# Kernel tuning notes

Hardware: AMD Instinct MI355X
Metric: run time of the kernel (lower is better)

The kernel has to match this reference:

```python
import jax, jax.numpy as jnp
import numpy as np

N_NODES = 100000
N_EDGES = 3200000
IN_FEATS = 128
HIDDEN = 8
HEADS = 4
OUT_FEATS = 1
NEG_SLOPE = 0.2


def setup_inputs() -> dict:
    key = jax.random.key(0)
    ks = jax.random.split(key, 12)
    x = jax.random.normal(ks[0], (N_NODES, IN_FEATS), dtype=jnp.float32)
    edge_index = jax.random.randint(ks[1], (2, N_EDGES), 0, N_NODES, dtype=jnp.int64)
    # conv1: in=128 -> heads=4, out=8 (concat)
    s1 = 1.0 / np.sqrt(IN_FEATS)
    W1 = jax.random.uniform(ks[2], (IN_FEATS, HEADS * HIDDEN), jnp.float32, -s1, s1)
    att_src1 = jax.random.normal(ks[3], (HEADS, HIDDEN), dtype=jnp.float32) * 0.1
    att_dst1 = jax.random.normal(ks[4], (HEADS, HIDDEN), dtype=jnp.float32) * 0.1
    b1 = jnp.zeros((HEADS * HIDDEN,), jnp.float32)
    # conv2: in=32 -> heads=1, out=1 (no concat)
    s2 = 1.0 / np.sqrt(HEADS * HIDDEN)
    W2 = jax.random.uniform(ks[5], (HEADS * HIDDEN, 1 * OUT_FEATS), jnp.float32, -s2, s2)
    att_src2 = jax.random.normal(ks[6], (1, OUT_FEATS), dtype=jnp.float32) * 0.1
    att_dst2 = jax.random.normal(ks[7], (1, OUT_FEATS), dtype=jnp.float32) * 0.1
    b2 = jnp.zeros((OUT_FEATS,), jnp.float32)
    return {"x": x, "edge_index": edge_index,
            "W1": W1, "att_src1": att_src1, "att_dst1": att_dst1, "b1": b1,
            "W2": W2, "att_src2": att_src2, "att_dst2": att_dst2, "b2": b2}


def gat_conv(x, src, dst, W, a_src, a_dst, b, heads, out_ch, concat):
    """PyG GATConv (eval mode: dropout identity), self-loops already included in src/dst."""
    N = x.shape[0]
    h = (x @ W).reshape(N, heads, out_ch)                 # [N,H,C]
    alpha_s = jnp.sum(h * a_src[None], axis=-1)           # [N,H]
    alpha_d = jnp.sum(h * a_dst[None], axis=-1)           # [N,H]
    e = jax.nn.leaky_relu(alpha_s[src] + alpha_d[dst], NEG_SLOPE)  # [E,H]
    # segment softmax over incoming edges per destination node
    m = jax.ops.segment_max(e, dst, num_segments=N)       # [N,H]; every node has a self-loop
    ex = jnp.exp(e - m[dst])
    denom = jax.ops.segment_sum(ex, dst, num_segments=N)
    alpha = ex / denom[dst]                               # [E,H]
    msg = alpha[:, :, None] * h[src]                      # [E,H,C]
    agg = jax.ops.segment_sum(msg, dst, num_segments=N)   # [N,H,C]
    if concat:
        agg = agg.reshape(N, heads * out_ch)
    else:
        agg = agg.mean(axis=1)
    return agg + b


def reference(x, edge_index, W1, att_src1, att_dst1, b1, W2, att_src2, att_dst2, b2):
    N = x.shape[0]
    loops = jnp.arange(N, dtype=edge_index.dtype)
    src = jnp.concatenate([edge_index[0], loops])
    dst = jnp.concatenate([edge_index[1], loops])
    h = gat_conv(x, src, dst, W1, att_src1, att_dst1, b1, HEADS, HIDDEN, True)
    h = jax.nn.elu(h)
    out = gat_conv(h, src, dst, W2, att_src2, att_dst2, b2, 1, OUT_FEATS, False)
    return out
```

## Files before the change

kernel.cpp:

```cpp
#include <hip/hip_runtime.h>
#include <hip/hip_fp16.h>

#define NEG_SLOPE 0.2f
#define LOG2E 1.4426950408889634f
#define NC 782
#define TILE 6144
#define CAP 4736

__device__ __forceinline__ int uclamp(int i, int n) {
    return ((unsigned)i < (unsigned)n) ? i : 0;
}


__global__ __launch_bounds__(512) void k_msplit(const int* __restrict__ ei, int* __restrict__ gcur,
                                                int* __restrict__ ebin, int E, int N) {
    __shared__ int hist[NC], lpre[NC], lcur[NC];
    __shared__ int tbuf[TILE];
    __shared__ unsigned short tcb[TILE];
    __shared__ int part[512];
    int t = threadIdx.x;
    int tb = blockIdx.x * TILE;
    int nt = E - tb; if (nt > TILE) nt = TILE; if (nt < 0) nt = 0;
    for (int i = t; i < NC; i += 512) { hist[i] = 0; lcur[i] = 0; }
    __syncthreads();
    int sv[12]; short cbv[12];
#pragma unroll
    for (int j = 0; j < 12; ++j) {
        int idx = tb + j * 512 + t;
        int cb = -1, v = 0;
        if (idx < E) {
            int s = uclamp(ei[idx], N), d = uclamp(ei[E + idx], N);
            cb = d >> 7;
            v = (s << 7) | (d & 127);
            atomicAdd(&hist[cb], 1);
        }
        sv[j] = v; cbv[j] = (short)cb;
    }
    __syncthreads();
    int i0 = 2 * t, i1 = 2 * t + 1;
    int h0 = (i0 < NC) ? hist[i0] : 0;
    int h1 = (i1 < NC) ? hist[i1] : 0;
    int a = h0 + h1;
    part[t] = a;
    __syncthreads();
    for (int off = 1; off < 512; off <<= 1) {
        int v = (t >= off) ? part[t - off] : 0;
        __syncthreads();
        part[t] += v;
        __syncthreads();
    }
    int excl = part[t] - a;
    if (i0 < NC) lpre[i0] = excl;
    if (i1 < NC) lpre[i1] = excl + h0;
    __syncthreads();
    for (int i = t; i < NC; i += 512) {
        int h = hist[i];
        if (h) hist[i] = atomicAdd(&gcur[i], h);
    }
    __syncthreads();
#pragma unroll
    for (int j = 0; j < 12; ++j) {
        int cb = cbv[j];
        if (cb >= 0) {
            int slot = lpre[cb] + atomicAdd(&lcur[cb], 1);
            tbuf[slot] = sv[j];
            tcb[slot] = (unsigned short)cb;
        }
    }
    __syncthreads();
    for (int i = t; i < nt; i += 512) {
        int cb = tcb[i];
        int pos = hist[cb] + (i - lpre[cb]);
        if (pos < (cb + 1) * CAP) ebin[pos] = tbuf[i];
    }
}


__global__ __launch_bounds__(512) void k_sortB(const int* __restrict__ gcur, int* __restrict__ ebin,
                                               int* __restrict__ rstart, int* __restrict__ rend,
                                               int N) {
    __shared__ int buf[CAP];
    __shared__ int cnt[128], pre[128], cur[128];
    __shared__ int part[128];
    int b = blockIdx.x, t = threadIdx.x;
    int p0 = b * CAP;
    int n = gcur[b] - p0;
    if (n < 0) n = 0; if (n > CAP) n = CAP;
    if (t < 128) { cnt[t] = 0; cur[t] = 0; }
    __syncthreads();
    for (int i = t; i < n; i += 512) {
        int v = ebin[p0 + i];
        buf[i] = v;
        atomicAdd(&cnt[v & 127], 1);
    }
    __syncthreads();
    if (t < 128) part[t] = cnt[t];
    __syncthreads();
    if (t < 128) {
        for (int off = 1; off < 128; off <<= 1) {
            int v = (t >= off) ? part[t - off] : 0;
            __syncthreads();
            part[t] += v;
            __syncthreads();
        }
    } else {
        for (int off = 1; off < 128; off <<= 1) { __syncthreads(); __syncthreads(); }
    }
    if (t < 128) {
        int a = cnt[t];
        pre[t] = part[t] - a;
        int d = (b << 7) + t;
        if (d < N) {
            rstart[d] = p0 + pre[t];
            rend[d]   = p0 + pre[t] + a;
        }
    }
    __syncthreads();
    for (int i = t; i < n; i += 512) {
        int v = buf[i];
        int dl = v & 127;
        int pos = p0 + pre[dl] + atomicAdd(&cur[dl], 1);
        ebin[pos] = v >> 7;
    }
}


__global__ __launch_bounds__(256) void k_node1(const float* __restrict__ x,
                                               const float* __restrict__ W1,
                                               const float* __restrict__ asw,
                                               const float* __restrict__ adw,
                                               __half* __restrict__ h1h,
                                               float* __restrict__ as1,
                                               float* __restrict__ ad1,
                                               int* __restrict__ gcur, int N) {
    __shared__ float Wl[128 * 32];
    __shared__ float xl[32 * 132];
    __shared__ float als[32], ald[32];
    int t = threadIdx.x;
    if (blockIdx.x < 4) {
        int gi = blockIdx.x * 256 + t;
        if (gi < NC) gcur[gi] = gi * CAP;
    }
    for (int i = t; i < 128 * 32; i += 256) Wl[i] = W1[i];
    if (t < 32) { als[t] = asw[t]; ald[t] = adw[t]; }
    int nbase = blockIdx.x * 32;
    for (int i = t; i < 1024; i += 256) {
        int nd = i >> 5, j = i & 31;
        int node = nbase + nd;
        float4 v = (node < N) ? ((const float4*)(x + (size_t)node * 128))[j]
                              : make_float4(0.f, 0.f, 0.f, 0.f);
        *(float4*)&xl[nd * 132 + j * 4] = v;
    }
    __syncthreads();
    int nl = t >> 3, cq = t & 7;
    int node = nbase + nl;
    float4 acc = make_float4(0.f, 0.f, 0.f, 0.f);
    const float* xr = &xl[nl * 132];
#pragma unroll 8
    for (int k = 0; k < 128; ++k) {
        float xv = xr[k];
        float4 w = *(const float4*)&Wl[k * 32 + cq * 4];
        acc.x += xv * w.x; acc.y += xv * w.y; acc.z += xv * w.z; acc.w += xv * w.w;
    }
    if (node < N) {
        __half2 ha = __floats2half2_rn(acc.x, acc.y);
        __half2 hb = __floats2half2_rn(acc.z, acc.w);
        uint2 u; u.x = *(unsigned*)&ha; u.y = *(unsigned*)&hb;
        ((uint2*)(h1h + (size_t)node * 32))[cq] = u;
        int c4 = cq * 4;
        float vs = acc.x * als[c4] + acc.y * als[c4 + 1] + acc.z * als[c4 + 2] + acc.w * als[c4 + 3];
        float vd = acc.x * ald[c4] + acc.y * ald[c4 + 1] + acc.z * ald[c4 + 2] + acc.w * ald[c4 + 3];
        vs += __shfl_xor(vs, 1);
        vd += __shfl_xor(vd, 1);
        if ((cq & 1) == 0) {
            as1[node * 4 + (cq >> 1)] = vs * LOG2E;
            ad1[node * 4 + (cq >> 1)] = vd * LOG2E;
        }
    }
}


__global__ __launch_bounds__(256) void k_aggr1(const int* __restrict__ rstart, const int* __restrict__ rend,
                                               const int* __restrict__ col,
                                               const __half* __restrict__ h1h,
                                               const float* __restrict__ as1, const float* __restrict__ ad1,
                                               const float* __restrict__ W2,
                                               float* __restrict__ g, int N) {
    int d = (blockIdx.x * 256 + threadIdx.x) >> 6;
    int lane = threadIdx.x & 63;
    if (d >= N) return;
    int slot = lane >> 2, q = lane & 3;
    float myAd = ad1[d * 4 + q];
    int p0 = rstart[d], p1 = rend[d];
    float acc[8];
#pragma unroll
    for (int i = 0; i < 8; ++i) acc[i] = 0.f;
    float ws = 0.f;
    int p = p0 + slot;
    while (p + 16 < p1) {
        int s0 = __builtin_nontemporal_load(&col[p]);
        int s1 = __builtin_nontemporal_load(&col[p + 16]);
        float av0 = as1[s0 * 4 + q];
        float av1 = as1[s1 * 4 + q];
        const __half* h0 = h1h + (size_t)s0 * 32 + q * 8;
        const __half* h1 = h1h + (size_t)s1 * 32 + q * 8;
        uint4 hv0 = *(const uint4*)h0;
        uint4 hv1 = *(const uint4*)h1;
        float e0 = av0 + myAd; e0 = e0 > 0.f ? e0 : NEG_SLOPE * e0;
        float e1 = av1 + myAd; e1 = e1 > 0.f ? e1 : NEG_SLOPE * e1;
        float w0 = exp2f(e0), w1 = exp2f(e1);
        ws += w0 + w1;
        const __half* a0p = (const __half*)&hv0;
        const __half* a1p = (const __half*)&hv1;
#pragma unroll
        for (int i = 0; i < 8; ++i) acc[i] += w0 * (float)a0p[i];
#pragma unroll
        for (int i = 0; i < 8; ++i) acc[i] += w1 * (float)a1p[i];
        p += 32;
    }
    if (p < p1) {
        int s = __builtin_nontemporal_load(&col[p]);
        float av = as1[s * 4 + q];
        uint4 hv = *(const uint4*)(h1h + (size_t)s * 32 + q * 8);
        float e = av + myAd; e = e > 0.f ? e : NEG_SLOPE * e;
        float w = exp2f(e);
        ws += w;
        const __half* ap = (const __half*)&hv;
#pragma unroll
        for (int i = 0; i < 8; ++i) acc[i] += w * (float)ap[i];
    }
#pragma unroll
    for (int m = 4; m <= 32; m <<= 1) {
        ws += __shfl_xor(ws, m);
#pragma unroll
        for (int i = 0; i < 8; ++i) acc[i] += __shfl_xor(acc[i], m);
    }
    {
        float e = as1[d * 4 + q] + myAd;
        e = e > 0.f ? e : NEG_SLOPE * e;
        float w = exp2f(e);
        uint4 hv = *(const uint4*)(h1h + (size_t)d * 32 + q * 8);
        ws += w;
        const __half* ap = (const __half*)&hv;
#pragma unroll
        for (int i = 0; i < 8; ++i) acc[i] += w * (float)ap[i];
    }
    float inv = 1.f / ws;
    float4 w2a = *(const float4*)(W2 + q * 8);
    float4 w2b = *(const float4*)(W2 + q * 8 + 4);
    float gv = 0.f;
#pragma unroll
    for (int i = 0; i < 8; ++i) {
        float val = acc[i] * inv;
        val = val > 0.f ? val : (__expf(val) - 1.f);
        float w2 = (i < 4) ? ((const float*)&w2a)[i] : ((const float*)&w2b)[i - 4];
        gv += val * w2;
    }
    gv += __shfl_xor(gv, 1);
    gv += __shfl_xor(gv, 2);
    if (lane == 0) g[d] = gv;
}


__global__ __launch_bounds__(256) void k_aggr2(const int* __restrict__ rstart, const int* __restrict__ rend,
                                               const int* __restrict__ col,
                                               const float* __restrict__ g,
                                               const float* __restrict__ asw,
                                               const float* __restrict__ adw,
                                               float* __restrict__ out, int N) {
    int tid = blockIdx.x * 256 + threadIdx.x;
    int d = tid >> 3, l = tid & 7;
    if (d >= N) return;
    float asc = asw[0] * LOG2E;
    float adc = adw[0] * LOG2E;
    float gd = g[d];
    float myd = gd * adc;
    int p0 = rstart[d], p1 = rend[d];
    float ws = 0.f, acc = 0.f;
    for (int p = p0 + l; p < p1; p += 8) {
        float gs = g[__builtin_nontemporal_load(&col[p])];
        float e = gs * asc + myd;
        e = e > 0.f ? e : NEG_SLOPE * e;
        float w = exp2f(e);
        ws += w;
        acc += w * gs;
    }
    ws += __shfl_xor(ws, 1); ws += __shfl_xor(ws, 2); ws += __shfl_xor(ws, 4);
    acc += __shfl_xor(acc, 1); acc += __shfl_xor(acc, 2); acc += __shfl_xor(acc, 4);
    if (l == 0) {
        float e = gd * asc + myd;
        e = e > 0.f ? e : NEG_SLOPE * e;
        float w = exp2f(e);
        ws += w;
        acc += w * gd;
        out[d] = acc / ws;
    }
}

extern "C" void kernel_launch(void* const* d_in, const int* in_sizes, int n_in,
                              void* d_out, int out_size, void* d_ws, size_t ws_size,
                              hipStream_t stream) {
    const float* x    = (const float*)d_in[0];
    const int*   ei   = (const int*)d_in[1];
    const float* W1   = (const float*)d_in[2];
    const float* as1w = (const float*)d_in[3];
    const float* ad1w = (const float*)d_in[4];
    const float* W2   = (const float*)d_in[6];
    const float* as2w = (const float*)d_in[7];
    const float* ad2w = (const float*)d_in[8];

    const int N  = in_sizes[0] / 128;
    const int E  = in_sizes[1] / 2;
    const int EB = NC * CAP;

    char* ws = (char*)d_ws;
    size_t off = 0;
    int*    gcur   = (int*)(ws + off);    off += 16384;
    int*    rstart = (int*)(ws + off);    off += (size_t)N * 4;
    int*    rend   = (int*)(ws + off);    off += (size_t)N * 4;
    int*    ebin   = (int*)(ws + off);    off += (size_t)EB * 4;
    __half* h1h    = (__half*)(ws + off); off += (size_t)N * 64;
    float*  as1    = (float*)(ws + off);  off += (size_t)N * 16;
    float*  ad1    = (float*)(ws + off);  off += (size_t)N * 16;
    float*  g      = (float*)(ws + off);  off += (size_t)N * 4;

    k_node1<<<(N + 31) / 32, 256, 0, stream>>>(x, W1, as1w, ad1w, h1h, as1, ad1, gcur, N);
    k_msplit<<<(E + TILE - 1) / TILE, 512, 0, stream>>>(ei, gcur, ebin, E, N);
    k_sortB<<<NC, 512, 0, stream>>>(gcur, ebin, rstart, rend, N);
    k_aggr1<<<(N + 3) / 4, 256, 0, stream>>>(rstart, rend, ebin, h1h, as1, ad1, W2, g, N);
    k_aggr2<<<(N * 8 + 255) / 256, 256, 0, stream>>>(rstart, rend, ebin, g, as2w, ad2w, (float*)d_out, N);
}
```

Baseline: 262.9 us.

## Split layer-1 aggregation into two head-pair passes with halved feature tables

Node features and attention scores are stored as two separate arrays, each holding two heads, and the first-layer aggregation runs as two kernel launches, one per head pair. Each launch accumulates into g, the second by adding to the first's result. The intent is a smaller gather working set per pass (3.2 MB of fp16 features instead of 6.4 MB) so random source-node gathers hit cache more often. The cost is reading the CSR column indices twice, an extra launch, and a read-modify-write of g.

```diff
diff --git a/kernel.cpp b/kernel.cpp
--- a/kernel.cpp
+++ b/kernel.cpp
@@ -129,9 +129,10 @@
                                                const float* __restrict__ W1,
                                                const float* __restrict__ asw,
                                                const float* __restrict__ adw,
-                                               __half* __restrict__ h1h,
-                                               float* __restrict__ as1,
-                                               float* __restrict__ ad1,
+                                               __half* __restrict__ hA,
+                                               __half* __restrict__ hB,
+                                               float* __restrict__ asA, float* __restrict__ asB,
+                                               float* __restrict__ adA, float* __restrict__ adB,
                                                int* __restrict__ gcur, int N) {
     __shared__ float Wl[128 * 32];
     __shared__ float xl[32 * 132];
@@ -166,31 +167,40 @@
         __half2 ha = __floats2half2_rn(acc.x, acc.y);
         __half2 hb = __floats2half2_rn(acc.z, acc.w);
         uint2 u; u.x = *(unsigned*)&ha; u.y = *(unsigned*)&hb;
-        ((uint2*)(h1h + (size_t)node * 32))[cq] = u;
+        __half* hT = (cq < 4) ? hA : hB;
+        ((uint2*)(hT + (size_t)node * 16))[cq & 3] = u;
         int c4 = cq * 4;
         float vs = acc.x * als[c4] + acc.y * als[c4 + 1] + acc.z * als[c4 + 2] + acc.w * als[c4 + 3];
         float vd = acc.x * ald[c4] + acc.y * ald[c4 + 1] + acc.z * ald[c4 + 2] + acc.w * ald[c4 + 3];
         vs += __shfl_xor(vs, 1);
         vd += __shfl_xor(vd, 1);
         if ((cq & 1) == 0) {
-            as1[node * 4 + (cq >> 1)] = vs * LOG2E;
-            ad1[node * 4 + (cq >> 1)] = vd * LOG2E;
-        }
-    }
-}
-
-
-__global__ __launch_bounds__(256) void k_aggr1(const int* __restrict__ rstart, const int* __restrict__ rend,
-                                               const int* __restrict__ col,
-                                               const __half* __restrict__ h1h,
-                                               const float* __restrict__ as1, const float* __restrict__ ad1,
-                                               const float* __restrict__ W2,
-                                               float* __restrict__ g, int N) {
-    int d = (blockIdx.x * 256 + threadIdx.x) >> 6;
+            int head = cq >> 1;
+            float* asT = (head < 2) ? asA : asB;
+            float* adT = (head < 2) ? adA : adB;
+            int hh = head & 1;
+            asT[node * 2 + hh] = vs * LOG2E;
+            adT[node * 2 + hh] = vd * LOG2E;
+        }
+    }
+}
+
+
+template<int ADD>
+__global__ __launch_bounds__(256) void k_aggr1h(const int* __restrict__ rstart, const int* __restrict__ rend,
+                                                const int* __restrict__ col,
+                                                const __half* __restrict__ hX,
+                                                const float* __restrict__ asX, const float* __restrict__ adX,
+                                                const float* __restrict__ W2h,
+                                                float* __restrict__ g, int N) {
+    int wid = (blockIdx.x * 256 + threadIdx.x) >> 6;
     int lane = threadIdx.x & 63;
+    int half = lane >> 5;
+    int d = wid * 2 + half;
     if (d >= N) return;
-    int slot = lane >> 2, q = lane & 3;
-    float myAd = ad1[d * 4 + q];
+    int slot = (lane >> 1) & 15;
+    int hq = lane & 1;
+    float myAd = adX[d * 2 + hq];
     int p0 = rstart[d], p1 = rend[d];
     float acc[8];
 #pragma unroll
@@ -200,14 +210,12 @@
     while (p + 16 < p1) {
         int s0 = __builtin_nontemporal_load(&col[p]);
         int s1 = __builtin_nontemporal_load(&col[p + 16]);
-        float av0 = as1[s0 * 4 + q];
-        float av1 = as1[s1 * 4 + q];
-        const __half* h0 = h1h + (size_t)s0 * 32 + q * 8;
-        const __half* h1 = h1h + (size_t)s1 * 32 + q * 8;
-        uint4 hv0 = *(const uint4*)h0;
-        uint4 hv1 = *(const uint4*)h1;
-        float e0 = av0 + myAd; e0 = e0 > 0.f ? e0 : NEG_SLOPE * e0;
-        float e1 = av1 + myAd; e1 = e1 > 0.f ? e1 : NEG_SLOPE * e1;
+        float a0 = asX[s0 * 2 + hq];
+        float a1 = asX[s1 * 2 + hq];
+        uint4 hv0 = *(const uint4*)(hX + (size_t)s0 * 16 + hq * 8);
+        uint4 hv1 = *(const uint4*)(hX + (size_t)s1 * 16 + hq * 8);
+        float e0 = a0 + myAd; e0 = e0 > 0.f ? e0 : NEG_SLOPE * e0;
+        float e1 = a1 + myAd; e1 = e1 > 0.f ? e1 : NEG_SLOPE * e1;
         float w0 = exp2f(e0), w1 = exp2f(e1);
         ws += w0 + w1;
         const __half* a0p = (const __half*)&hv0;
@@ -218,36 +226,37 @@
         for (int i = 0; i < 8; ++i) acc[i] += w1 * (float)a1p[i];
         p += 32;
     }
-    if (p < p1) {
+    while (p < p1) {
         int s = __builtin_nontemporal_load(&col[p]);
-        float av = as1[s * 4 + q];
-        uint4 hv = *(const uint4*)(h1h + (size_t)s * 32 + q * 8);
+        float av = asX[s * 2 + hq];
+        uint4 hv = *(const uint4*)(hX + (size_t)s * 16 + hq * 8);
         float e = av + myAd; e = e > 0.f ? e : NEG_SLOPE * e;
         float w = exp2f(e);
         ws += w;
         const __half* ap = (const __half*)&hv;
 #pragma unroll
         for (int i = 0; i < 8; ++i) acc[i] += w * (float)ap[i];
-    }
-#pragma unroll
-    for (int m = 4; m <= 32; m <<= 1) {
+        p += 16;
+    }
+#pragma unroll
+    for (int m = 2; m <= 16; m <<= 1) {
         ws += __shfl_xor(ws, m);
 #pragma unroll
         for (int i = 0; i < 8; ++i) acc[i] += __shfl_xor(acc[i], m);
     }
     {
-        float e = as1[d * 4 + q] + myAd;
+        float e = asX[d * 2 + hq] + myAd;
         e = e > 0.f ? e : NEG_SLOPE * e;
         float w = exp2f(e);
-        uint4 hv = *(const uint4*)(h1h + (size_t)d * 32 + q * 8);
+        uint4 hv = *(const uint4*)(hX + (size_t)d * 16 + hq * 8);
         ws += w;
         const __half* ap = (const __half*)&hv;
 #pragma unroll
         for (int i = 0; i < 8; ++i) acc[i] += w * (float)ap[i];
     }
     float inv = 1.f / ws;
-    float4 w2a = *(const float4*)(W2 + q * 8);
-    float4 w2b = *(const float4*)(W2 + q * 8 + 4);
+    float4 w2a = *(const float4*)(W2h + hq * 8);
+    float4 w2b = *(const float4*)(W2h + hq * 8 + 4);
     float gv = 0.f;
 #pragma unroll
     for (int i = 0; i < 8; ++i) {
@@ -257,8 +266,9 @@
         gv += val * w2;
     }
     gv += __shfl_xor(gv, 1);
-    gv += __shfl_xor(gv, 2);
-    if (lane == 0) g[d] = gv;
+    if ((lane & 31) == 0) {
+        if (ADD) g[d] += gv; else g[d] = gv;
+    }
 }
 
 
@@ -319,14 +329,18 @@
     int*    rstart = (int*)(ws + off);    off += (size_t)N * 4;
     int*    rend   = (int*)(ws + off);    off += (size_t)N * 4;
     int*    ebin   = (int*)(ws + off);    off += (size_t)EB * 4;
-    __half* h1h    = (__half*)(ws + off); off += (size_t)N * 64;
-    float*  as1    = (float*)(ws + off);  off += (size_t)N * 16;
-    float*  ad1    = (float*)(ws + off);  off += (size_t)N * 16;
+    __half* hA     = (__half*)(ws + off); off += (size_t)N * 32;
+    __half* hB     = (__half*)(ws + off); off += (size_t)N * 32;
+    float*  asA    = (float*)(ws + off);  off += (size_t)N * 8;
+    float*  asB    = (float*)(ws + off);  off += (size_t)N * 8;
+    float*  adA    = (float*)(ws + off);  off += (size_t)N * 8;
+    float*  adB    = (float*)(ws + off);  off += (size_t)N * 8;
     float*  g      = (float*)(ws + off);  off += (size_t)N * 4;
 
-    k_node1<<<(N + 31) / 32, 256, 0, stream>>>(x, W1, as1w, ad1w, h1h, as1, ad1, gcur, N);
+    k_node1<<<(N + 31) / 32, 256, 0, stream>>>(x, W1, as1w, ad1w, hA, hB, asA, asB, adA, adB, gcur, N);
     k_msplit<<<(E + TILE - 1) / TILE, 512, 0, stream>>>(ei, gcur, ebin, E, N);
     k_sortB<<<NC, 512, 0, stream>>>(gcur, ebin, rstart, rend, N);
-    k_aggr1<<<(N + 3) / 4, 256, 0, stream>>>(rstart, rend, ebin, h1h, as1, ad1, W2, g, N);
+    k_aggr1h<0><<<(N + 7) / 8, 256, 0, stream>>>(rstart, rend, ebin, hA, asA, adA, W2,      g, N);
+    k_aggr1h<1><<<(N + 7) / 8, 256, 0, stream>>>(rstart, rend, ebin, hB, asB, adB, W2 + 16, g, N);
     k_aggr2<<<(N * 8 + 255) / 256, 256, 0, stream>>>(rstart, rend, ebin, g, as2w, ad2w, (float*)d_out, N);
 }
```

New measurement: 285.2 us. 1.08x slower.

## Recompute source attention logits from fp16 features and use half-wave per node

Applied to the files above, without the earlier changes.

The per-node source attention logit array is no longer written by the node kernel. The aggregation kernel instead recomputes it per edge as a dot product of the gathered fp16 features with the attention weights, which removes one random gather per edge and the as1 buffer. The aggregation also moves from one wavefront per destination node to half a wavefront (32 lanes) per node, so each node uses 8 edge slots and grid size doubles in nodes per block. The cost is extra ALU work per edge and logits computed from half-precision features, which slightly changes numerics.

```diff
diff --git a/kernel.cpp b/kernel.cpp
--- a/kernel.cpp
+++ b/kernel.cpp
@@ -127,22 +127,20 @@
 
 __global__ __launch_bounds__(256) void k_node1(const float* __restrict__ x,
                                                const float* __restrict__ W1,
-                                               const float* __restrict__ asw,
                                                const float* __restrict__ adw,
                                                __half* __restrict__ h1h,
-                                               float* __restrict__ as1,
                                                float* __restrict__ ad1,
                                                int* __restrict__ gcur, int N) {
     __shared__ float Wl[128 * 32];
     __shared__ float xl[32 * 132];
-    __shared__ float als[32], ald[32];
+    __shared__ float ald[32];
     int t = threadIdx.x;
     if (blockIdx.x < 4) {
         int gi = blockIdx.x * 256 + t;
         if (gi < NC) gcur[gi] = gi * CAP;
     }
     for (int i = t; i < 128 * 32; i += 256) Wl[i] = W1[i];
-    if (t < 32) { als[t] = asw[t]; ald[t] = adw[t]; }
+    if (t < 32) ald[t] = adw[t];
     int nbase = blockIdx.x * 32;
     for (int i = t; i < 1024; i += 256) {
         int nd = i >> 5, j = i & 31;
@@ -168,12 +166,9 @@
         uint2 u; u.x = *(unsigned*)&ha; u.y = *(unsigned*)&hb;
         ((uint2*)(h1h + (size_t)node * 32))[cq] = u;
         int c4 = cq * 4;
-        float vs = acc.x * als[c4] + acc.y * als[c4 + 1] + acc.z * als[c4 + 2] + acc.w * als[c4 + 3];
         float vd = acc.x * ald[c4] + acc.y * ald[c4 + 1] + acc.z * ald[c4 + 2] + acc.w * ald[c4 + 3];
-        vs += __shfl_xor(vs, 1);
         vd += __shfl_xor(vd, 1);
         if ((cq & 1) == 0) {
-            as1[node * 4 + (cq >> 1)] = vs * LOG2E;
             ad1[node * 4 + (cq >> 1)] = vd * LOG2E;
         }
     }
@@ -183,13 +178,22 @@
 __global__ __launch_bounds__(256) void k_aggr1(const int* __restrict__ rstart, const int* __restrict__ rend,
                                                const int* __restrict__ col,
                                                const __half* __restrict__ h1h,
-                                               const float* __restrict__ as1, const float* __restrict__ ad1,
+                                               const float* __restrict__ ad1,
+                                               const float* __restrict__ asw,
                                                const float* __restrict__ W2,
                                                float* __restrict__ g, int N) {
-    int d = (blockIdx.x * 256 + threadIdx.x) >> 6;
+    int wid = (blockIdx.x * 256 + threadIdx.x) >> 6;
     int lane = threadIdx.x & 63;
+    int half = lane >> 5;
+    int d = wid * 2 + half;
     if (d >= N) return;
-    int slot = lane >> 2, q = lane & 3;
+    int l5 = lane & 31;
+    int slot = l5 >> 2;
+    int q = lane & 3;
+    float4 aA = *(const float4*)(asw + q * 8);
+    float4 aB = *(const float4*)(asw + q * 8 + 4);
+    float as0 = aA.x * LOG2E, as1 = aA.y * LOG2E, as2 = aA.z * LOG2E, as3 = aA.w * LOG2E;
+    float as4 = aB.x * LOG2E, as5 = aB.y * LOG2E, as6 = aB.z * LOG2E, as7 = aB.w * LOG2E;
     float myAd = ad1[d * 4 + q];
     int p0 = rstart[d], p1 = rend[d];
     float acc[8];
@@ -197,54 +201,51 @@
     for (int i = 0; i < 8; ++i) acc[i] = 0.f;
     float ws = 0.f;
     int p = p0 + slot;
-    while (p + 16 < p1) {
+#define DOT8(hp) (as0*(float)(hp)[0] + as1*(float)(hp)[1] + as2*(float)(hp)[2] + as3*(float)(hp)[3] \
+                + as4*(float)(hp)[4] + as5*(float)(hp)[5] + as6*(float)(hp)[6] + as7*(float)(hp)[7])
+    while (p + 8 < p1) {
         int s0 = __builtin_nontemporal_load(&col[p]);
-        int s1 = __builtin_nontemporal_load(&col[p + 16]);
-        float av0 = as1[s0 * 4 + q];
-        float av1 = as1[s1 * 4 + q];
-        const __half* h0 = h1h + (size_t)s0 * 32 + q * 8;
-        const __half* h1 = h1h + (size_t)s1 * 32 + q * 8;
-        uint4 hv0 = *(const uint4*)h0;
-        uint4 hv1 = *(const uint4*)h1;
-        float e0 = av0 + myAd; e0 = e0 > 0.f ? e0 : NEG_SLOPE * e0;
-        float e1 = av1 + myAd; e1 = e1 > 0.f ? e1 : NEG_SLOPE * e1;
+        int s1 = __builtin_nontemporal_load(&col[p + 8]);
+        uint4 hv0 = *(const uint4*)(h1h + (size_t)s0 * 32 + q * 8);
+        uint4 hv1 = *(const uint4*)(h1h + (size_t)s1 * 32 + q * 8);
+        const __half* a0p = (const __half*)&hv0;
+        const __half* a1p = (const __half*)&hv1;
+        float e0 = DOT8(a0p) + myAd; e0 = e0 > 0.f ? e0 : NEG_SLOPE * e0;
+        float e1 = DOT8(a1p) + myAd; e1 = e1 > 0.f ? e1 : NEG_SLOPE * e1;
         float w0 = exp2f(e0), w1 = exp2f(e1);
         ws += w0 + w1;
-        const __half* a0p = (const __half*)&hv0;
-        const __half* a1p = (const __half*)&hv1;
 #pragma unroll
         for (int i = 0; i < 8; ++i) acc[i] += w0 * (float)a0p[i];
 #pragma unroll
         for (int i = 0; i < 8; ++i) acc[i] += w1 * (float)a1p[i];
-        p += 32;
+        p += 16;
     }
     if (p < p1) {
         int s = __builtin_nontemporal_load(&col[p]);
-        float av = as1[s * 4 + q];
         uint4 hv = *(const uint4*)(h1h + (size_t)s * 32 + q * 8);
-        float e = av + myAd; e = e > 0.f ? e : NEG_SLOPE * e;
+        const __half* ap = (const __half*)&hv;
+        float e = DOT8(ap) + myAd; e = e > 0.f ? e : NEG_SLOPE * e;
         float w = exp2f(e);
         ws += w;
+#pragma unroll
+        for (int i = 0; i < 8; ++i) acc[i] += w * (float)ap[i];
+    }
+#pragma unroll
+    for (int m = 4; m <= 16; m <<= 1) {
+        ws += __shfl_xor(ws, m);
+#pragma unroll
+        for (int i = 0; i < 8; ++i) acc[i] += __shfl_xor(acc[i], m);
+    }
+    {
+        uint4 hv = *(const uint4*)(h1h + (size_t)d * 32 + q * 8);
         const __half* ap = (const __half*)&hv;
+        float e = DOT8(ap) + myAd; e = e > 0.f ? e : NEG_SLOPE * e;
+        float w = exp2f(e);
+        ws += w;
 #pragma unroll
         for (int i = 0; i < 8; ++i) acc[i] += w * (float)ap[i];
     }
-#pragma unroll
-    for (int m = 4; m <= 32; m <<= 1) {
-        ws += __shfl_xor(ws, m);
-#pragma unroll
-        for (int i = 0; i < 8; ++i) acc[i] += __shfl_xor(acc[i], m);
-    }
-    {
-        float e = as1[d * 4 + q] + myAd;
-        e = e > 0.f ? e : NEG_SLOPE * e;
-        float w = exp2f(e);
-        uint4 hv = *(const uint4*)(h1h + (size_t)d * 32 + q * 8);
-        ws += w;
-        const __half* ap = (const __half*)&hv;
-#pragma unroll
-        for (int i = 0; i < 8; ++i) acc[i] += w * (float)ap[i];
-    }
+#undef DOT8
     float inv = 1.f / ws;
     float4 w2a = *(const float4*)(W2 + q * 8);
     float4 w2b = *(const float4*)(W2 + q * 8 + 4);
@@ -258,7 +259,7 @@
     }
     gv += __shfl_xor(gv, 1);
     gv += __shfl_xor(gv, 2);
-    if (lane == 0) g[d] = gv;
+    if (l5 == 0) g[d] = gv;
 }
 
 
@@ -320,13 +321,12 @@
     int*    rend   = (int*)(ws + off);    off += (size_t)N * 4;
     int*    ebin   = (int*)(ws + off);    off += (size_t)EB * 4;
     __half* h1h    = (__half*)(ws + off); off += (size_t)N * 64;
-    float*  as1    = (float*)(ws + off);  off += (size_t)N * 16;
     float*  ad1    = (float*)(ws + off);  off += (size_t)N * 16;
     float*  g      = (float*)(ws + off);  off += (size_t)N * 4;
 
-    k_node1<<<(N + 31) / 32, 256, 0, stream>>>(x, W1, as1w, ad1w, h1h, as1, ad1, gcur, N);
+    k_node1<<<(N + 31) / 32, 256, 0, stream>>>(x, W1, ad1w, h1h, ad1, gcur, N);
     k_msplit<<<(E + TILE - 1) / TILE, 512, 0, stream>>>(ei, gcur, ebin, E, N);
     k_sortB<<<NC, 512, 0, stream>>>(gcur, ebin, rstart, rend, N);
-    k_aggr1<<<(N + 3) / 4, 256, 0, stream>>>(rstart, rend, ebin, h1h, as1, ad1, W2, g, N);
+    k_aggr1<<<(N + 7) / 8, 256, 0, stream>>>(rstart, rend, ebin, h1h, ad1, as1w, W2, g, N);
     k_aggr2<<<(N * 8 + 255) / 256, 256, 0, stream>>>(rstart, rend, ebin, g, as2w, ad2w, (float*)d_out, N);
 }
```

New measurement: 247.1 us. -6.0%, faster.
